# Kernel tuning notes

Measured on AMD Instinct MI355X. Metric: run time of the kernel, lower is better.

The kernel has to match this reference:

```python
import jax, jax.numpy as jnp
import numpy as np
import math

NH, NKV, D = 32, 8, 128  # heads, kv heads, head dim

def _alibi_slopes(n):
    cp2 = 2 ** math.floor(math.log2(n))
    base = 2.0 ** (-8.0 / cp2)
    slopes = base ** np.arange(1, cp2 + 1, dtype=np.float32)
    if cp2 != n:
        extra_base = 2.0 ** (-4.0 / cp2)
        extra = extra_base ** np.arange(1, 1 + 2 * (n - cp2), 2, dtype=np.float32)
        slopes = np.concatenate([slopes, extra])
    return slopes.astype(np.float32)

def setup_inputs() -> dict:
    key = jax.random.key(0)
    k1, k2, k3 = jax.random.split(key, 3)
    B, S, H = 4, 1024, 4096
    qkv_out = NH * D + 2 * NKV * D  # 6144
    return {
        "hidden_states": jax.random.normal(k1, (B, S, H), jnp.float32) * 0.02,
        "w_qkv": jax.random.normal(k2, (H, qkv_out), jnp.float32) * 0.02,
        "w_o": jax.random.normal(k3, (NH * D, H), jnp.float32) * 0.02,
    }

def reference(hidden_states, w_qkv, w_o):
    B, S, H = hidden_states.shape
    G = NH // NKV  # query groups per kv head
    scale = D ** -0.5

    qkv = hidden_states @ w_qkv  # [B,S,6144]
    q = qkv[..., : NH * D].reshape(B, S, NKV, G, D)
    k = qkv[..., NH * D : NH * D + NKV * D].reshape(B, S, NKV, D)
    v = qkv[..., NH * D + NKV * D :].reshape(B, S, NKV, D)

    scores = jnp.einsum("bqhgd,bkhd->bhgqk", q, k) * scale  # [B,NKV,G,S,S]

    slopes = jnp.asarray(_alibi_slopes(NH)).reshape(NKV, G)  # head order
    pos = jnp.arange(S)
    rel = pos[:, None] - pos[None, :]  # i - j
    sqrt_dist = jnp.sqrt(jnp.maximum(rel, 0).astype(jnp.float32))
    bias = -slopes[:, :, None, None] * sqrt_dist  # ALiBi-sqrt bias
    bias = jnp.where(rel[None, None] >= 0, bias, -jnp.inf)  # causal mask

    attn = jax.nn.softmax(scores + bias[None], axis=-1)
    out = jnp.einsum("bhgqk,bkhd->bqhgd", attn, v).reshape(B, S, NH * D)
    return out @ w_o
```

## Files before the change

kernel.cpp:

```cpp
#include <hip/hip_runtime.h>
#include <stdint.h>

typedef __attribute__((ext_vector_type(4))) float floatx4;
typedef __attribute__((ext_vector_type(8))) short short8;
typedef unsigned short ushort_t;

#define DEVI __device__ __forceinline__

constexpr int Bc   = 4;
constexpr int Sc   = 1024;
constexpr int Hc   = 4096;
constexpr int NHc  = 32;
constexpr int NKVc = 8;
constexpr int Dc   = 128;
constexpr int QKVO = 6144;
constexpr int Mc   = Bc * Sc;

DEVI ushort_t f2bf(float f) {
  union { float f; unsigned u; } x; x.f = f;
  unsigned u = x.u;
  u += 0x7fffu + ((u >> 16) & 1u);
  return (ushort_t)(u >> 16);
}

DEVI short8 cvt8(floatx4 a, floatx4 b) {
  short8 r;
  r[0] = (short)f2bf(a[0]); r[1] = (short)f2bf(a[1]);
  r[2] = (short)f2bf(a[2]); r[3] = (short)f2bf(a[3]);
  r[4] = (short)f2bf(b[0]); r[5] = (short)f2bf(b[1]);
  r[6] = (short)f2bf(b[2]); r[7] = (short)f2bf(b[3]);
  return r;
}

DEVI void load_lds16(const ushort_t* g, ushort_t* l) {
  __builtin_amdgcn_global_load_lds(
      (const __attribute__((address_space(1))) void*)g,
      (__attribute__((address_space(3))) void*)l, 16, 0, 0);
}

#define BARRIER()  asm volatile("s_barrier" ::: "memory")
#define LGKM0()    asm volatile("s_waitcnt lgkmcnt(0)" ::: "memory")
#define VMCNT(n)   asm volatile("s_waitcnt vmcnt(" #n ")" ::: "memory")

__global__ __launch_bounds__(256)
void cvt_bf16(const float* __restrict__ src, ushort_t* __restrict__ dst, int n8)
{
  const int i = blockIdx.x * 256 + threadIdx.x;
  if (i >= n8) return;
  const floatx4 f0 = *(const floatx4*)(src + (size_t)i * 8);
  const floatx4 f1 = *(const floatx4*)(src + (size_t)i * 8 + 4);
  *(short8*)(dst + (size_t)i * 8) = cvt8(f0, f1);
}

__global__ __launch_bounds__(256)
void transpose_cvt(const float* __restrict__ src, ushort_t* __restrict__ dst,
                   int R, int C)
{
  __shared__ float ts[64][67];
  const int cb = C >> 6;
  const int r0 = (blockIdx.x / cb) << 6;
  const int c0 = (blockIdx.x % cb) << 6;
  const int t  = threadIdx.x;

  const int lr = t >> 4, lc = (t & 15) << 2;
#pragma unroll
  for (int i = 0; i < 4; ++i) {
    const floatx4 v = *(const floatx4*)(src + (size_t)(r0 + lr + 16 * i) * C + c0 + lc);
#pragma unroll
    for (int j = 0; j < 4; ++j) ts[lr + 16 * i][lc + j] = v[j];
  }
  __syncthreads();

  const int c     = ((t >> 6) << 4) + ((t & 63) >> 2);
  const int chunk = t & 3;
  short8 t0, t1;
#pragma unroll
  for (int k = 0; k < 8; ++k) t0[k] = (short)f2bf(ts[chunk * 16 + k][c]);
#pragma unroll
  for (int k = 0; k < 8; ++k) t1[k] = (short)f2bf(ts[chunk * 16 + 8 + k][c]);
  ushort_t* dp = dst + (size_t)(c0 + c) * R + r0 + chunk * 16;
  *(short8*)dp       = t0;
  *(short8*)(dp + 8) = t1;
}

__global__ __launch_bounds__(256)
void v_transpose(const ushort_t* __restrict__ qkv, ushort_t* __restrict__ vt)
{
  __shared__ ushort_t ts[64][72];
  const int bid = blockIdx.x;
  const int db  = bid & 1;
  const int sb  = (bid >> 1) & 15;
  const int hkv = (bid >> 5) & 7;
  const int b   = bid >> 8;
  const int t   = threadIdx.x;

  const ushort_t* src = qkv + (size_t)(b * Sc + sb * 64) * QKVO
                        + (NHc * Dc + NKVc * Dc) + hkv * Dc + db * 64;
  const int lr = t >> 3, lc = (t & 7) * 8;
  *(short8*)&ts[lr][lc]      = *(const short8*)(src + (size_t)lr * QKVO + lc);
  *(short8*)&ts[lr + 32][lc] = *(const short8*)(src + (size_t)(lr + 32) * QKVO + lc);
  __syncthreads();

  ushort_t* dst = vt + ((size_t)(b * NKVc + hkv) * Dc + db * 64) * Sc + sb * 64;
  const int dr  = t >> 2;
  const int sc0 = (t & 3) * 16;
  short8 o0, o1;
#pragma unroll
  for (int k = 0; k < 8; ++k) o0[k] = (short)ts[sc0 + k][dr];
#pragma unroll
  for (int k = 0; k < 8; ++k) o1[k] = (short)ts[sc0 + 8 + k][dr];
  *(short8*)(dst + (size_t)dr * Sc + sc0)     = o0;
  *(short8*)(dst + (size_t)dr * Sc + sc0 + 8) = o1;
}

template<int NFRAG, bool OBF16>
__global__ __launch_bounds__(512, 2)
void gemm_nt8(const ushort_t* __restrict__ A, const ushort_t* __restrict__ BT,
              void* __restrict__ Cp, int M, int N, int K)
{
  constexpr int BN = 64 * NFRAG;
  __shared__ __align__(16) ushort_t As[2][256 * 64];
  __shared__ __align__(16) ushort_t Bs[2][BN * 64];

  const int nb  = N / BN;
  const int nwg = (M >> 8) * nb;
  int bid = blockIdx.x;
  bid = (bid & 7) * (nwg >> 3) + (bid >> 3);
  const int bm = bid / nb, bn = bid % nb;
  const int m0 = bm << 8, n0 = bn * BN;

  const int tid  = threadIdx.x;
  const int wid  = tid >> 6, lane = tid & 63;
  const int wm   = wid >> 2, wn = wid & 3;
  const int fr   = lane & 15;
  const int g16  = (lane >> 4) << 4;
  const int rsw  = (fr & 7) << 4;
  const int l8   = lane >> 3;
  const int scol = ((lane & 7) ^ l8) << 3;

  const int sr   = (wid << 3);
  const size_t Ks = (size_t)K;
  const ushort_t* agS = A  + (size_t)(m0 + sr + l8) * K + scol;
  const ushort_t* bgS = BT + (size_t)(n0 + sr + l8) * K + scol;

  const int rowA = (wm * 128 + fr) * 128;
  const int rowB = (wn * 16 * NFRAG + fr) * 128;
  const int cb0  = g16 ^ rsw;
  const int cb1  = (64 + g16) ^ rsw;

  const floatx4 fz = {0.f, 0.f, 0.f, 0.f};
  floatx4 acc[8][NFRAG];
#pragma unroll
  for (int i = 0; i < 8; ++i)
#pragma unroll
    for (int f = 0; f < NFRAG; ++f) acc[i][f] = fz;

  auto STB = [&](int v, size_t kn) {
#pragma unroll
    for (int j = 0; j < NFRAG; ++j)
      load_lds16(bgS + (size_t)(64 * j) * Ks + kn, &Bs[v][(sr + 64 * j) * 64]);
  };
  auto STA = [&](int v, size_t kn) {
    load_lds16(agS + kn,            &As[v][(sr +   0) * 64]);
    load_lds16(agS + 128 * Ks + kn, &As[v][(sr + 128) * 64]);
    load_lds16(agS +  64 * Ks + kn, &As[v][(sr +  64) * 64]);
    load_lds16(agS + 192 * Ks + kn, &As[v][(sr + 192) * 64]);
  };

  STB(0, 0); STA(0, 0);
  VMCNT(2);
  BARRIER();

  const int NT = K >> 6;
  for (int kt = 0; kt < NT; ++kt) {
    const int u = kt & 1, v = u ^ 1;
    const char* Au = (const char*)&As[u][0];
    const char* Bu = (const char*)&Bs[u][0];
    const bool st  = (kt + 1 < NT);
    const size_t kn = (size_t)(kt + 1) << 6;

#define LDA(i, ks) (*(const short8*)(Au + rowA + (i) * 2048 + ((ks) ? cb1 : cb0)))
#define LDB(f, ks) (*(const short8*)(Bu + rowB + (f) * 2048 + ((ks) ? cb1 : cb0)))

    short8 aR[4], bR[NFRAG];

#pragma unroll
    for (int i = 0; i < 4; ++i) aR[i] = LDA(i, 0);
#pragma unroll
    for (int f = 0; f < NFRAG; ++f) bR[f] = LDB(f, 0);
    if (st) {
      STB(v, kn);
      if constexpr (NFRAG == 4) { VMCNT(4); } else { VMCNT(3); }
    } else { VMCNT(0); }
    BARRIER();
    LGKM0(); __builtin_amdgcn_sched_barrier(0);
    __builtin_amdgcn_s_setprio(1);
#pragma unroll
    for (int i = 0; i < 4; ++i)
#pragma unroll
      for (int f = 0; f < NFRAG; ++f)
        acc[i][f] = __builtin_amdgcn_mfma_f32_16x16x32_bf16(aR[i], bR[f], acc[i][f], 0, 0, 0);
    __builtin_amdgcn_s_setprio(0);
    BARRIER();

#pragma unroll
    for (int i = 0; i < 4; ++i) aR[i] = LDA(4 + i, 0);
    if (st) STA(v, kn);
    BARRIER();
    LGKM0(); __builtin_amdgcn_sched_barrier(0);
    __builtin_amdgcn_s_setprio(1);
#pragma unroll
    for (int i = 0; i < 4; ++i)
#pragma unroll
      for (int f = 0; f < NFRAG; ++f)
        acc[4 + i][f] = __builtin_amdgcn_mfma_f32_16x16x32_bf16(aR[i], bR[f], acc[4 + i][f], 0, 0, 0);
    __builtin_amdgcn_s_setprio(0);
    BARRIER();

#pragma unroll
    for (int i = 0; i < 4; ++i) aR[i] = LDA(4 + i, 1);
#pragma unroll
    for (int f = 0; f < NFRAG; ++f) bR[f] = LDB(f, 1);
    BARRIER();
    LGKM0(); __builtin_amdgcn_sched_barrier(0);
    __builtin_amdgcn_s_setprio(1);
#pragma unroll
    for (int i = 0; i < 4; ++i)
#pragma unroll
      for (int f = 0; f < NFRAG; ++f)
        acc[4 + i][f] = __builtin_amdgcn_mfma_f32_16x16x32_bf16(aR[i], bR[f], acc[4 + i][f], 0, 0, 0);
    __builtin_amdgcn_s_setprio(0);
    BARRIER();

#pragma unroll
    for (int i = 0; i < 4; ++i) aR[i] = LDA(i, 1);
    if (st) { VMCNT(2); }
    BARRIER();
    LGKM0(); __builtin_amdgcn_sched_barrier(0);
    __builtin_amdgcn_s_setprio(1);
#pragma unroll
    for (int i = 0; i < 4; ++i)
#pragma unroll
      for (int f = 0; f < NFRAG; ++f)
        acc[i][f] = __builtin_amdgcn_mfma_f32_16x16x32_bf16(aR[i], bR[f], acc[i][f], 0, 0, 0);
    __builtin_amdgcn_s_setprio(0);
    BARRIER();

#undef LDA
#undef LDB
  }

  const int r4 = (lane >> 4) << 2;
#pragma unroll
  for (int i = 0; i < 8; ++i) {
#pragma unroll
    for (int rr = 0; rr < 4; ++rr) {
      const size_t row = (size_t)(m0 + wm * 128 + i * 16 + r4 + rr);
#pragma unroll
      for (int f = 0; f < NFRAG; ++f) {
        const size_t col = (size_t)(n0 + wn * 16 * NFRAG + f * 16 + fr);
        if constexpr (OBF16)
          ((ushort_t*)Cp)[row * N + col] = f2bf(acc[i][f][rr]);
        else
          ((float*)Cp)[row * N + col] = acc[i][f][rr];
      }
    }
  }
}

__global__ __launch_bounds__(256, 2)
void attn_fwd(const ushort_t* __restrict__ qkv,
              const ushort_t* __restrict__ vt,
              ushort_t* __restrict__ attn)
{
  __shared__ __align__(16) ushort_t Plds[4][32 * 40];

  const int bid = blockIdx.x;
  const int x   = bid & 7;
  const int p   = bid >> 3;
  const int j   = p & 15;
  const int g   = ((p >> 4) << 3) + x;
  const int b   = g >> 3;
  const int hkv = g & 7;

  const int tid  = threadIdx.x;
  const int wid  = tid >> 6, lane = tid & 63;
  const int h    = hkv * 4 + wid;
  const int fr   = lane & 15;
  const int kk8  = (lane >> 4) << 3;
  const int q4   = (lane >> 4) << 2;
  const float slope = exp2f(-0.25f * (float)(h + 1));
  const float scale = 0.08838834764831845f;

  const ushort_t* qp  = qkv + (size_t)b * Sc * QKVO + (size_t)h * Dc;
  const ushort_t* kp  = qkv + (size_t)b * Sc * QKVO + NHc * Dc + (size_t)hkv * Dc;
  const ushort_t* vtp = vt + (size_t)(b * NKVc + hkv) * Dc * Sc;
  ushort_t* myP = &Plds[wid][0];

  const floatx4 fz = {0.f, 0.f, 0.f, 0.f};

  auto process = [&](const int qb) {
    short8 qf[2][4];
#pragma unroll
    for (int t = 0; t < 2; ++t) {
      const int qrow = qb * 32 + t * 16 + fr;
#pragma unroll
      for (int s = 0; s < 4; ++s)
        qf[t][s] = *(const short8*)(qp + (size_t)qrow * QKVO + s * 32 + kk8);
    }

    floatx4 o[2][8];
#pragma unroll
    for (int t = 0; t < 2; ++t)
#pragma unroll
      for (int jj = 0; jj < 8; ++jj) o[t][jj] = fz;
    float mrow[2][4], lrow[2][4];
#pragma unroll
    for (int t = 0; t < 2; ++t)
#pragma unroll
      for (int rr = 0; rr < 4; ++rr) { mrow[t][rr] = -1e30f; lrow[t][rr] = 0.f; }

    for (int kb = 0; kb <= qb; ++kb) {
      floatx4 s_[2][2];
      s_[0][0] = fz; s_[0][1] = fz; s_[1][0] = fz; s_[1][1] = fz;
#pragma unroll
      for (int half = 0; half < 2; ++half) {
        const int kcol = kb * 32 + half * 16 + fr;
#pragma unroll
        for (int s = 0; s < 4; ++s) {
          const short8 kf = *(const short8*)(kp + (size_t)kcol * QKVO + s * 32 + kk8);
          s_[0][half] = __builtin_amdgcn_mfma_f32_16x16x32_bf16(qf[0][s], kf, s_[0][half], 0, 0, 0);
          s_[1][half] = __builtin_amdgcn_mfma_f32_16x16x32_bf16(qf[1][s], kf, s_[1][half], 0, 0, 0);
        }
      }

      short8 vf[8];
#pragma unroll
      for (int jj = 0; jj < 8; ++jj)
        vf[jj] = *(const short8*)(vtp + (size_t)(jj * 16 + fr) * Sc + kb * 32 + kk8);

#pragma unroll
      for (int t = 0; t < 2; ++t)
#pragma unroll
        for (int rr = 0; rr < 4; ++rr) {
          const int qg  = qb * 32 + t * 16 + q4 + rr;
          const int dk0 = qg - (kb * 32 + fr);
          const int dk1 = dk0 - 16;
          s_[t][0][rr] = (dk0 >= 0)
              ? s_[t][0][rr] * scale - slope * sqrtf((float)dk0) : -1e30f;
          s_[t][1][rr] = (dk1 >= 0)
              ? s_[t][1][rr] * scale - slope * sqrtf((float)dk1) : -1e30f;
        }

      float pmv[2][4];
#pragma unroll
      for (int t = 0; t < 2; ++t)
#pragma unroll
        for (int rr = 0; rr < 4; ++rr) {
          float pm = fmaxf(s_[t][0][rr], s_[t][1][rr]);
#pragma unroll
          for (int m = 1; m < 16; m <<= 1) pm = fmaxf(pm, __shfl_xor(pm, m));
          pmv[t][rr] = pm;
        }

      int need = 0;
#pragma unroll
      for (int t = 0; t < 2; ++t)
#pragma unroll
        for (int rr = 0; rr < 4; ++rr)
          need |= (pmv[t][rr] > mrow[t][rr] + 8.f) ? 1 : 0;
      if (__any(need)) {
#pragma unroll
        for (int t = 0; t < 2; ++t)
#pragma unroll
          for (int rr = 0; rr < 4; ++rr) {
            const float mnew = fmaxf(mrow[t][rr], pmv[t][rr]);
            const float corr = __expf(mrow[t][rr] - mnew);
            lrow[t][rr] *= corr;
            mrow[t][rr] = mnew;
#pragma unroll
            for (int jj = 0; jj < 8; ++jj) o[t][jj][rr] *= corr;
          }
      }

#pragma unroll
      for (int t = 0; t < 2; ++t)
#pragma unroll
        for (int rr = 0; rr < 4; ++rr) {
          const float p0 = __expf(s_[t][0][rr] - mrow[t][rr]);
          const float p1 = __expf(s_[t][1][rr] - mrow[t][rr]);
          lrow[t][rr] += p0 + p1;
          myP[(t * 16 + q4 + rr) * 40 + fr]      = f2bf(p0);
          myP[(t * 16 + q4 + rr) * 40 + 16 + fr] = f2bf(p1);
        }
      short8 pa[2];
      pa[0] = *(const short8*)&myP[fr * 40 + kk8];
      pa[1] = *(const short8*)&myP[(16 + fr) * 40 + kk8];

#pragma unroll
      for (int jj = 0; jj < 8; ++jj) {
        o[0][jj] = __builtin_amdgcn_mfma_f32_16x16x32_bf16(pa[0], vf[jj], o[0][jj], 0, 0, 0);
        o[1][jj] = __builtin_amdgcn_mfma_f32_16x16x32_bf16(pa[1], vf[jj], o[1][jj], 0, 0, 0);
      }
    }

#pragma unroll
    for (int t = 0; t < 2; ++t)
#pragma unroll
      for (int rr = 0; rr < 4; ++rr) {
        float rs = lrow[t][rr];
#pragma unroll
        for (int m = 1; m < 16; m <<= 1) rs += __shfl_xor(rs, m);
        const float inv = 1.f / rs;
        const size_t tok = (size_t)b * Sc + qb * 32 + t * 16 + q4 + rr;
#pragma unroll
        for (int jj = 0; jj < 8; ++jj)
          attn[tok * (size_t)(NHc * Dc) + h * Dc + jj * 16 + fr] = f2bf(o[t][jj][rr] * inv);
      }
  };

  process(31 - j);
  process(j);
}

extern "C" void kernel_launch(void* const* d_in, const int* in_sizes, int n_in,
                              void* d_out, int out_size, void* d_ws, size_t ws_size,
                              hipStream_t stream)
{
  const float* hidden = (const float*)d_in[0];
  const float* w_qkv  = (const float*)d_in[1];
  const float* w_o    = (const float*)d_in[2];
  float* out = (float*)d_out;

  ushort_t* wqT   = (ushort_t*)d_ws;
  ushort_t* hidb  = wqT + (size_t)QKVO * Hc;
  ushort_t* qkvb  = hidb + (size_t)Mc * Hc;
  ushort_t* attnb = hidb;
  ushort_t* woT   = wqT;
  ushort_t* vtb   = wqT + (size_t)Mc * Hc;

  cvt_bf16<<<dim3((Mc * Hc / 8) / 256), dim3(256), 0, stream>>>(
      hidden, hidb, Mc * Hc / 8);
  transpose_cvt<<<dim3((Hc / 64) * (QKVO / 64)), dim3(256), 0, stream>>>(
      w_qkv, wqT, Hc, QKVO);
  gemm_nt8<3, true><<<dim3((Mc / 256) * (QKVO / 192)), dim3(512), 0, stream>>>(
      hidb, wqT, qkvb, Mc, QKVO, Hc);
  v_transpose<<<dim3(1024), dim3(256), 0, stream>>>(qkvb, vtb);
  attn_fwd<<<dim3(512), dim3(256), 0, stream>>>(qkvb, vtb, attnb);
  transpose_cvt<<<dim3((Hc / 64) * (Hc / 64)), dim3(256), 0, stream>>>(
      w_o, woT, Hc, Hc);
  gemm_nt8<4, false><<<dim3((Mc / 256) * (Hc / 256)), dim3(512), 0, stream>>>(
      attnb, woT, out, Mc, Hc, Hc);
}
```

Baseline: 594.5 us.

## Restructure GEMM mainloop to consume two K-tiles per iteration with staggered prefetch

The bf16 GEMM main loop now processes two 64-wide K tiles per iteration, one from each LDS buffer. B fragments for both tiles and both k-halves are held in registers, and the global-to-LDS loads for the next pair of tiles are split into quarter chunks spread across eight MFMA phases. The aim is to hide global load latency better and cut LDS reload traffic for B. In exchange it raises register pressure under the 512-thread, 2-block launch bounds, which risks spills or lower occupancy, and the hand-tuned vmcnt waits are harder to get right.

```diff
diff --git a/kernel.cpp b/kernel.cpp
--- a/kernel.cpp
+++ b/kernel.cpp
@@ -115,8 +115,8 @@
 
 template<int NFRAG, bool OBF16>
 __global__ __launch_bounds__(512, 2)
-void gemm_nt8(const ushort_t* __restrict__ A, const ushort_t* __restrict__ BT,
-              void* __restrict__ Cp, int M, int N, int K)
+void gemm_nt8d(const ushort_t* __restrict__ A, const ushort_t* __restrict__ BT,
+               void* __restrict__ Cp, int M, int N, int K)
 {
   constexpr int BN = 64 * NFRAG;
   __shared__ __align__(16) ushort_t As[2][256 * 64];
@@ -155,100 +155,127 @@
 #pragma unroll
     for (int f = 0; f < NFRAG; ++f) acc[i][f] = fz;
 
-  auto STB = [&](int v, size_t kn) {
-#pragma unroll
-    for (int j = 0; j < NFRAG; ++j)
-      load_lds16(bgS + (size_t)(64 * j) * Ks + kn, &Bs[v][(sr + 64 * j) * 64]);
+  auto SAq0 = [&](int s, size_t kn) {
+    load_lds16(agS + kn,            &As[s][(sr +   0) * 64]);
+    load_lds16(agS + 128 * Ks + kn, &As[s][(sr + 128) * 64]);
   };
-  auto STA = [&](int v, size_t kn) {
-    load_lds16(agS + kn,            &As[v][(sr +   0) * 64]);
-    load_lds16(agS + 128 * Ks + kn, &As[v][(sr + 128) * 64]);
-    load_lds16(agS +  64 * Ks + kn, &As[v][(sr +  64) * 64]);
-    load_lds16(agS + 192 * Ks + kn, &As[v][(sr + 192) * 64]);
+  auto SAq1 = [&](int s, size_t kn) {
+    load_lds16(agS +  64 * Ks + kn, &As[s][(sr +  64) * 64]);
+    load_lds16(agS + 192 * Ks + kn, &As[s][(sr + 192) * 64]);
   };
-
-  STB(0, 0); STA(0, 0);
-  VMCNT(2);
+  auto SB01 = [&](int s, size_t kn) {
+    load_lds16(bgS + kn,            &Bs[s][(sr +   0) * 64]);
+    load_lds16(bgS +  64 * Ks + kn, &Bs[s][(sr +  64) * 64]);
+  };
+  auto SB2 = [&](int s, size_t kn) {
+    load_lds16(bgS + 128 * Ks + kn, &Bs[s][(sr + 128) * 64]);
+    if constexpr (NFRAG == 4)
+      load_lds16(bgS + 192 * Ks + kn, &Bs[s][(sr + 192) * 64]);
+  };
+
+  SAq0(0, 0); SAq1(0, 0); SB01(0, 0); SB2(0, 0);
+  SAq0(1, 64); SB01(1, 64); SB2(1, 64);
+  VMCNT(0);
   BARRIER();
 
-  const int NT = K >> 6;
-  for (int kt = 0; kt < NT; ++kt) {
-    const int u = kt & 1, v = u ^ 1;
-    const char* Au = (const char*)&As[u][0];
-    const char* Bu = (const char*)&Bs[u][0];
-    const bool st  = (kt + 1 < NT);
-    const size_t kn = (size_t)(kt + 1) << 6;
-
-#define LDA(i, ks) (*(const short8*)(Au + rowA + (i) * 2048 + ((ks) ? cb1 : cb0)))
-#define LDB(f, ks) (*(const short8*)(Bu + rowB + (f) * 2048 + ((ks) ? cb1 : cb0)))
-
-    short8 aR[4], bR[NFRAG];
-
-#pragma unroll
-    for (int i = 0; i < 4; ++i) aR[i] = LDA(i, 0);
-#pragma unroll
-    for (int f = 0; f < NFRAG; ++f) bR[f] = LDB(f, 0);
-    if (st) {
-      STB(v, kn);
-      if constexpr (NFRAG == 4) { VMCNT(4); } else { VMCNT(3); }
-    } else { VMCNT(0); }
-    BARRIER();
-    LGKM0(); __builtin_amdgcn_sched_barrier(0);
-    __builtin_amdgcn_s_setprio(1);
-#pragma unroll
-    for (int i = 0; i < 4; ++i)
-#pragma unroll
-      for (int f = 0; f < NFRAG; ++f)
-        acc[i][f] = __builtin_amdgcn_mfma_f32_16x16x32_bf16(aR[i], bR[f], acc[i][f], 0, 0, 0);
+#define LDA(s, i, ks) (*(const short8*)((const char*)&As[s][0] + rowA + (i) * 2048 + ((ks) ? cb1 : cb0)))
+#define LDB(s, f, ks) (*(const short8*)((const char*)&Bs[s][0] + rowB + (f) * 2048 + ((ks) ? cb1 : cb0)))
+
+  const int NI = K >> 7;
+  for (int it = 0; it < NI; ++it) {
+    const size_t kt0 = (size_t)it << 7;
+    const size_t k1 = kt0 + 64, k2 = kt0 + 128, k3 = kt0 + 192;
+    const bool st2 = (it + 1 < NI);
+    const bool st3 = st2;
+
+    short8 aR[4], bR[NFRAG][2], bS[NFRAG][2];
+
+#define MFMA_PH(base, barr, ks)                                              \
+    __builtin_amdgcn_s_setprio(1);                                          \
+    _Pragma("unroll")                                                       \
+    for (int i = 0; i < 4; ++i)                                             \
+      _Pragma("unroll")                                                     \
+      for (int f = 0; f < NFRAG; ++f)                                       \
+        acc[(base) + i][f] = __builtin_amdgcn_mfma_f32_16x16x32_bf16(       \
+            aR[i], barr[f][ks], acc[(base) + i][f], 0, 0, 0);               \
     __builtin_amdgcn_s_setprio(0);
-    BARRIER();
-
-#pragma unroll
-    for (int i = 0; i < 4; ++i) aR[i] = LDA(4 + i, 0);
-    if (st) STA(v, kn);
-    BARRIER();
-    LGKM0(); __builtin_amdgcn_sched_barrier(0);
-    __builtin_amdgcn_s_setprio(1);
-#pragma unroll
-    for (int i = 0; i < 4; ++i)
-#pragma unroll
-      for (int f = 0; f < NFRAG; ++f)
-        acc[4 + i][f] = __builtin_amdgcn_mfma_f32_16x16x32_bf16(aR[i], bR[f], acc[4 + i][f], 0, 0, 0);
-    __builtin_amdgcn_s_setprio(0);
-    BARRIER();
-
-#pragma unroll
-    for (int i = 0; i < 4; ++i) aR[i] = LDA(4 + i, 1);
-#pragma unroll
-    for (int f = 0; f < NFRAG; ++f) bR[f] = LDB(f, 1);
-    BARRIER();
-    LGKM0(); __builtin_amdgcn_sched_barrier(0);
-    __builtin_amdgcn_s_setprio(1);
-#pragma unroll
-    for (int i = 0; i < 4; ++i)
-#pragma unroll
-      for (int f = 0; f < NFRAG; ++f)
-        acc[4 + i][f] = __builtin_amdgcn_mfma_f32_16x16x32_bf16(aR[i], bR[f], acc[4 + i][f], 0, 0, 0);
-    __builtin_amdgcn_s_setprio(0);
-    BARRIER();
-
-#pragma unroll
-    for (int i = 0; i < 4; ++i) aR[i] = LDA(i, 1);
-    if (st) { VMCNT(2); }
-    BARRIER();
-    LGKM0(); __builtin_amdgcn_sched_barrier(0);
-    __builtin_amdgcn_s_setprio(1);
-#pragma unroll
-    for (int i = 0; i < 4; ++i)
-#pragma unroll
-      for (int f = 0; f < NFRAG; ++f)
-        acc[i][f] = __builtin_amdgcn_mfma_f32_16x16x32_bf16(aR[i], bR[f], acc[i][f], 0, 0, 0);
-    __builtin_amdgcn_s_setprio(0);
-    BARRIER();
-
+
+#pragma unroll
+    for (int i = 0; i < 4; ++i) aR[i] = LDA(0, i, 0);
+#pragma unroll
+    for (int f = 0; f < NFRAG; ++f) { bR[f][0] = LDB(0, f, 0); bR[f][1] = LDB(0, f, 1); }
+    SAq1(1, k1);
+    VMCNT(4);
+    BARRIER();
+    LGKM0(); __builtin_amdgcn_sched_barrier(0);
+    MFMA_PH(0, bR, 0)
+    BARRIER();
+
+#pragma unroll
+    for (int i = 0; i < 4; ++i) aR[i] = LDA(1, i, 0);
+#pragma unroll
+    for (int f = 0; f < NFRAG; ++f) { bS[f][0] = LDB(1, f, 0); bS[f][1] = LDB(1, f, 1); }
+    if (st2) SB01(0, k2);
+    VMCNT(4);
+    BARRIER();
+    LGKM0(); __builtin_amdgcn_sched_barrier(0);
+    MFMA_PH(0, bS, 0)
+    BARRIER();
+
+#pragma unroll
+    for (int i = 0; i < 4; ++i) aR[i] = LDA(0, 4 + i, 0);
+    if (st2) SB2(0, k2);
+    if constexpr (NFRAG == 4) { VMCNT(4); } else { VMCNT(3); }
+    BARRIER();
+    LGKM0(); __builtin_amdgcn_sched_barrier(0);
+    MFMA_PH(4, bR, 0)
+    BARRIER();
+
+#pragma unroll
+    for (int i = 0; i < 4; ++i) aR[i] = LDA(1, 4 + i, 0);
+    if (st3) SB01(1, k3);
+    BARRIER();
+    LGKM0(); __builtin_amdgcn_sched_barrier(0);
+    MFMA_PH(4, bS, 0)
+    BARRIER();
+
+#pragma unroll
+    for (int i = 0; i < 4; ++i) aR[i] = LDA(0, i, 1);
+    if (st3) SB2(1, k3);
+    BARRIER();
+    LGKM0(); __builtin_amdgcn_sched_barrier(0);
+    MFMA_PH(0, bR, 1)
+    BARRIER();
+
+#pragma unroll
+    for (int i = 0; i < 4; ++i) aR[i] = LDA(1, i, 1);
+    if (st2) SAq0(0, k2);
+    BARRIER();
+    LGKM0(); __builtin_amdgcn_sched_barrier(0);
+    MFMA_PH(0, bS, 1)
+    BARRIER();
+
+#pragma unroll
+    for (int i = 0; i < 4; ++i) aR[i] = LDA(0, 4 + i, 1);
+    if (st3) SAq0(1, k3);
+    BARRIER();
+    LGKM0(); __builtin_amdgcn_sched_barrier(0);
+    MFMA_PH(4, bR, 1)
+    BARRIER();
+
+#pragma unroll
+    for (int i = 0; i < 4; ++i) aR[i] = LDA(1, 4 + i, 1);
+    if (st2) SAq1(0, k2);
+    VMCNT(4);
+    BARRIER();
+    LGKM0(); __builtin_amdgcn_sched_barrier(0);
+    MFMA_PH(4, bS, 1)
+    BARRIER();
+
+#undef MFMA_PH
+  }
 #undef LDA
 #undef LDB
-  }
 
   const int r4 = (lane >> 4) << 2;
 #pragma unroll
@@ -443,12 +470,12 @@
       hidden, hidb, Mc * Hc / 8);
   transpose_cvt<<<dim3((Hc / 64) * (QKVO / 64)), dim3(256), 0, stream>>>(
       w_qkv, wqT, Hc, QKVO);
-  gemm_nt8<3, true><<<dim3((Mc / 256) * (QKVO / 192)), dim3(512), 0, stream>>>(
+  gemm_nt8d<3, true><<<dim3((Mc / 256) * (QKVO / 192)), dim3(512), 0, stream>>>(
       hidb, wqT, qkvb, Mc, QKVO, Hc);
   v_transpose<<<dim3(1024), dim3(256), 0, stream>>>(qkvb, vtb);
   attn_fwd<<<dim3(512), dim3(256), 0, stream>>>(qkvb, vtb, attnb);
   transpose_cvt<<<dim3((Hc / 64) * (Hc / 64)), dim3(256), 0, stream>>>(
       w_o, woT, Hc, Hc);
-  gemm_nt8<4, false><<<dim3((Mc / 256) * (Hc / 256)), dim3(512), 0, stream>>>(
+  gemm_nt8d<4, false><<<dim3((Mc / 256) * (Hc / 256)), dim3(512), 0, stream>>>(
       attnb, woT, out, Mc, Hc, Hc);
 }
```

Measured after the change: 619.8 us. +4.3%, slower.
